# Optimization experiments

Measured on AMD Instinct MI355X. Metric: run time of the kernel, lower is better.

The kernel has to match this reference:

```python
import jax, jax.numpy as jnp
import numpy as np

LN_EPS = 1e-5  # torch nn.LayerNorm default


def layernorm(x, g, b):
    mu = jnp.mean(x, axis=-1, keepdims=True)
    var = jnp.var(x, axis=-1, keepdims=True)
    return (x - mu) * jax.lax.rsqrt(var + LN_EPS) * g + b


def setup_inputs() -> dict:
    key = jax.random.key(0)
    ks = jax.random.split(key, 12)
    B, N, Dn, Dm, E, L = 4, 20000, 64, 128, 160000, 2
    inp = {}
    inp["node_feat"] = jax.random.normal(ks[0], (B, N, Dn), jnp.float32)
    inp["in_W"] = jax.random.normal(ks[1], (Dn, Dm), jnp.float32) * 0.1
    inp["in_b"] = jnp.zeros((Dm,), jnp.float32)
    inp["node_W"] = jax.random.normal(ks[2], (L, 3, Dm, Dm), jnp.float32) * 0.05
    inp["node_b"] = jnp.zeros((L, 3, Dm), jnp.float32)
    inp["edge_W"] = jax.random.normal(ks[3], (L, 2, 16, Dm), jnp.float32) * 0.1
    inp["edge_b"] = jnp.zeros((L, 2, Dm), jnp.float32)
    inp["ln_g"] = jnp.ones((L, Dm), jnp.float32)
    inp["ln_b"] = jnp.zeros((L, Dm), jnp.float32)
    inp["ea0"] = jax.random.normal(ks[4], (E, 16), jnp.float32)
    inp["ea1"] = jax.random.normal(ks[5], (E, 16), jnp.float32)
    inp["ei0"] = jax.random.randint(ks[6], (2, E), 0, N)
    inp["ei1"] = jax.random.randint(ks[7], (2, E), 0, N)
    inp["ei2"] = jax.random.randint(ks[8], (2, E), 0, N)
    return inp


def reference(node_feat, in_W, in_b, node_W, node_b, edge_W, edge_b, ln_g, ln_b,
              ea0, ea1, ei0, ei1, ei2):
    # input projection: [B,N,Dn] -> [B,N,Dm]
    H = node_feat @ in_W + in_b
    edge_idx = [ei0, ei1, ei2]
    edge_attr = [ea0, ea1, None]  # relation 2 has edge_attr_dims == 0 (Identity/skip)
    n_layers = node_W.shape[0]
    for l in range(n_layers):
        agg = jnp.zeros_like(H)
        for r in range(3):
            src, dst = edge_idx[r][0], edge_idx[r][1]
            # gather src nodes per batch then per-relation linear: [B,E,Dm]
            msg = H[:, src] @ node_W[l, r] + node_b[l, r]
            if edge_attr[r] is not None:
                # edge attrs shared across batch -> broadcast add
                msg = msg + (edge_attr[r] @ edge_W[l, r] + edge_b[l, r])[None]
            # scatter-add messages to dst nodes, batched
            agg = agg.at[:, dst].add(msg)
        H = layernorm(H + jax.nn.relu(agg), ln_g[l], ln_b[l])
    return H
```

## Files before the change

### kernel.cpp

```cpp
#include <hip/hip_runtime.h>


#define NNODES 20000
#define NB     4
#define BROWS  (NB * NNODES)
#define DN     64
#define DM     128
#define NE     160000
#define CAP    64
#define LN_EPS 1e-5f
#define KE     448
#define LDW    88

typedef __attribute__((ext_vector_type(8))) short bf16x8;
typedef __attribute__((ext_vector_type(4))) float f32x4;
typedef __attribute__((ext_vector_type(2))) float f32x2;
typedef __attribute__((ext_vector_type(8))) unsigned short u16x8;

__device__ inline float bf2f(unsigned short u) {
    union { unsigned int i; float f; } x; x.i = ((unsigned int)u) << 16; return x.f;
}
__device__ inline unsigned short f2bf(float f) {
    union { float f; unsigned int i; } x; x.f = f;
    unsigned int r = x.i + 0x7FFFu + ((x.i >> 16) & 1u);
    return (unsigned short)(r >> 16);
}
__device__ inline f32x2 bfpair(unsigned int w) {
    union { unsigned int u; float f; } lo, hi;
    lo.u = w << 16; hi.u = w & 0xffff0000u;
    return (f32x2){lo.f, hi.f};
}

__global__ void k_scatter(const int* __restrict__ ei0, const int* __restrict__ ei1,
                          const int* __restrict__ ei2, int* __restrict__ cursor,
                          int* __restrict__ srcs, int* __restrict__ eids) {
    int tid = blockIdx.x * blockDim.x + threadIdx.x;
    if (tid >= 3 * NE) return;
    int r = tid / NE, e = tid - r * NE;
    const int* ei = (r == 0) ? ei0 : ((r == 1) ? ei1 : ei2);
    int src = ei[e], dst = ei[NE + e];
    int p = atomicAdd(&cursor[r * NNODES + dst], 1);
    if (p < CAP) {
        srcs[(r * NNODES + dst) * CAP + p] = src << 8;
        if (r < 2) eids[(r * NNODES + dst) * CAP + p] = e;
    }
}

__global__ __launch_bounds__(256) void k_sgather(const int* __restrict__ deg,
                                                 const int* __restrict__ eids,
                                                 const float* __restrict__ ea0,
                                                 const float* __restrict__ ea1,
                                                 float* __restrict__ S) {
    int task = blockIdx.x * 4 + (threadIdx.x >> 6);
    int r = task / NNODES;
    const float* ea = r ? ea1 : ea0;
    int lane = threadIdx.x & 63;
    int k = lane & 15, sub = lane >> 4;
    int dg = deg[task]; if (dg > CAP) dg = CAP;
    const int* bk = eids + (size_t)task * CAP;
    float acc = 0.f;
    for (int j = sub; j < dg; j += 4) {
        int e = bk[j];
        acc += ea[e * 16 + k];
    }
    acc += __shfl_xor(acc, 16, 64);
    acc += __shfl_xor(acc, 32, 64);
    if (lane < 16) S[(size_t)task * 16 + k] = acc;
}

__global__ __launch_bounds__(256) void k_wprep(const float* __restrict__ nW,
                                               const float* __restrict__ nb,
                                               const float* __restrict__ eW,
                                               const float* __restrict__ eb,
                                               const float* __restrict__ inW,
                                               unsigned short* __restrict__ Wt,
                                               unsigned short* __restrict__ Wp) {
    int lin = blockIdx.x * 256 + threadIdx.x;
    if (lin < 2 * 128 * KE) {
        int l = lin / (128 * KE);
        int rem = lin - l * 128 * KE;
        int n = rem / KE, k = rem - n * KE;
        float v;
        if (k < 384) {
            int r = k >> 7, kk = k & 127;
            v = nW[(((size_t)(l * 3 + r) * 128) + kk) * 128 + n];
        } else {
            int e = k - 384;
            if (e < 3) {
                v = nb[(l * 3 + e) * DM + n];
                if (e < 2) v += eb[(l * 2 + e) * DM + n];
            } else if (e < 35) {
                int r2 = (e - 3) >> 4, j = (e - 3) & 15;
                v = eW[((size_t)((l * 2 + r2) * 16 + j)) * DM + n];
            } else v = 0.f;
        }
        Wt[lin] = f2bf(v);
    } else {
        int i = lin - 2 * 128 * KE;
        int n = i >> 6, k = i & 63;
        Wp[n * 64 + k] = f2bf(inW[(size_t)k * DM + n]);
    }
}

__global__ __launch_bounds__(256) void k_proj(const float* __restrict__ X,
                                              const unsigned short* __restrict__ Wp,
                                              const float* __restrict__ bias,
                                              unsigned short* __restrict__ HB) {
    __shared__ __align__(16) unsigned short As[64][LDW];
    __shared__ __align__(16) unsigned short Bs[128][LDW];
    int t = threadIdx.x;
    int m0 = blockIdx.x * 64;
#pragma unroll
    for (int i = 0; i < 4; ++i) {
        int lin = t + 256 * i;
        int row = lin >> 4, seg = lin & 15;
        float4 v = *(const float4*)(X + (size_t)(m0 + row) * DN + seg * 4);
        ushort4 h; h.x = f2bf(v.x); h.y = f2bf(v.y); h.z = f2bf(v.z); h.w = f2bf(v.w);
        *(ushort4*)&As[row][seg * 4] = h;
    }
#pragma unroll
    for (int i = 0; i < 4; ++i) {
        int lin = t + 256 * i;
        int row = lin >> 3, seg = lin & 7;
        *(uint4*)&Bs[row][seg * 8] = *(const uint4*)(Wp + (size_t)row * 64 + seg * 8);
    }
    __syncthreads();
    int w = t >> 6, lane = t & 63;
    int q = lane >> 4, lm = lane & 15;
    f32x4 acc[8];
#pragma unroll
    for (int ct = 0; ct < 8; ++ct) acc[ct] = (f32x4){0.f, 0.f, 0.f, 0.f};
#pragma unroll
    for (int kt = 0; kt < 2; ++kt) {
        bf16x8 a = *(const bf16x8*)&As[w * 16 + lm][kt * 32 + q * 8];
#pragma unroll
        for (int ct = 0; ct < 8; ++ct) {
            bf16x8 bf = *(const bf16x8*)&Bs[ct * 16 + lm][kt * 32 + q * 8];
            acc[ct] = __builtin_amdgcn_mfma_f32_16x16x32_bf16(a, bf, acc[ct], 0, 0, 0);
        }
    }
#pragma unroll
    for (int reg = 0; reg < 4; ++reg) {
        int row = m0 + w * 16 + q * 4 + reg;
#pragma unroll
        for (int ct = 0; ct < 8; ++ct) {
            int col = ct * 16 + lm;
            HB[(size_t)row * DM + col] = f2bf(acc[ct][reg] + bias[col]);
        }
    }
}

__device__ inline uint4 ld16(const char* __restrict__ base, unsigned off) {
    return *(const uint4*)(base + off);
}
__device__ inline void acc4(f32x2* a, uint4 p0, uint4 p1, uint4 p2, uint4 p3) {
    a[0] += (bfpair(p0.x) + bfpair(p1.x)) + (bfpair(p2.x) + bfpair(p3.x));
    a[1] += (bfpair(p0.y) + bfpair(p1.y)) + (bfpair(p2.y) + bfpair(p3.y));
    a[2] += (bfpair(p0.z) + bfpair(p1.z)) + (bfpair(p2.z) + bfpair(p3.z));
    a[3] += (bfpair(p0.w) + bfpair(p1.w)) + (bfpair(p2.w) + bfpair(p3.w));
}

__device__ inline void gather_rel(const char* __restrict__ HbB, unsigned c16,
                                  const int* __restrict__ bk, int dg, f32x2* a) {
#pragma unroll
    for (int i = 0; i < 4; ++i) a[i] = (f32x2){0.f, 0.f};
    int nb = dg >> 2;
    int j = nb << 2;
    if (nb > 0) {
        int4 s = *(const int4*)bk;
        uint4 p0 = ld16(HbB, (unsigned)s.x + c16);
        uint4 p1 = ld16(HbB, (unsigned)s.y + c16);
        uint4 p2 = ld16(HbB, (unsigned)s.z + c16);
        uint4 p3 = ld16(HbB, (unsigned)s.w + c16);
        for (int b = 1; b < nb; ++b) {
            int4 s2 = *(const int4*)(bk + (b << 2));
            uint4 q0 = ld16(HbB, (unsigned)s2.x + c16);
            uint4 q1 = ld16(HbB, (unsigned)s2.y + c16);
            uint4 q2 = ld16(HbB, (unsigned)s2.z + c16);
            uint4 q3 = ld16(HbB, (unsigned)s2.w + c16);
            acc4(a, p0, p1, p2, p3);
            p0 = q0; p1 = q1; p2 = q2; p3 = q3;
        }
        acc4(a, p0, p1, p2, p3);
    }
    for (; j < dg; ++j) {
        uint4 u = ld16(HbB, (unsigned)bk[j] + c16);
        a[0] += bfpair(u.x); a[1] += bfpair(u.y);
        a[2] += bfpair(u.z); a[3] += bfpair(u.w);
    }
}

__global__ __launch_bounds__(256) void k_spmm(const unsigned short* __restrict__ HB,
                                              const int* __restrict__ deg,
                                              const int* __restrict__ srcs,
                                              const float* __restrict__ S,
                                              unsigned short* __restrict__ G) {
    int blk = blockIdx.x;
    int s = blk & 7;
    int bb = s >> 1;
    int idx = ((blk >> 3) << 1) + (s & 1);
    int n0 = idx * 16;
    int g = threadIdx.x >> 4, lane = threadIdx.x & 15;
    int n = n0 + g;
    unsigned c16 = (unsigned)lane * 16;
    const char* HbB = (const char*)HB + (size_t)bb * NNODES * DM * 2;
    size_t rowbase = ((size_t)(bb * NNODES + n)) * KE;

    int dt0 = deg[n], dt1 = deg[NNODES + n], dt2 = deg[2 * NNODES + n];
    const int* bk0 = srcs + (size_t)n * CAP;
    const int* bk1 = bk0 + (size_t)NNODES * CAP;
    const int* bk2 = bk1 + (size_t)NNODES * CAP;

    f32x2 a[4];
    u16x8 o;

    gather_rel(HbB, c16, bk0, dt0 > CAP ? CAP : dt0, a);
#pragma unroll
    for (int i = 0; i < 4; ++i) { o[2 * i] = f2bf(a[i].x); o[2 * i + 1] = f2bf(a[i].y); }
    *(u16x8*)(G + rowbase + 0 * 128 + lane * 8) = o;

    gather_rel(HbB, c16, bk1, dt1 > CAP ? CAP : dt1, a);
#pragma unroll
    for (int i = 0; i < 4; ++i) { o[2 * i] = f2bf(a[i].x); o[2 * i + 1] = f2bf(a[i].y); }
    *(u16x8*)(G + rowbase + 1 * 128 + lane * 8) = o;

    gather_rel(HbB, c16, bk2, dt2 > CAP ? CAP : dt2, a);
#pragma unroll
    for (int i = 0; i < 4; ++i) { o[2 * i] = f2bf(a[i].x); o[2 * i + 1] = f2bf(a[i].y); }
    *(u16x8*)(G + rowbase + 2 * 128 + lane * 8) = o;

    if (lane < 8) {
        int dt[3] = {dt0, dt1, dt2};
        u16x8 e;
#pragma unroll
        for (int j = 0; j < 8; ++j) {
            int kk = lane * 8 + j;
            float v;
            if (kk < 3)       v = (float)dt[kk];
            else if (kk < 19) v = S[((size_t)(0 * NNODES + n)) * 16 + (kk - 3)];
            else if (kk < 35) v = S[((size_t)(1 * NNODES + n)) * 16 + (kk - 19)];
            else              v = 0.f;
            e[j] = f2bf(v);
        }
        *(u16x8*)(G + rowbase + 384 + lane * 8) = e;
    }
}

__global__ __launch_bounds__(256) void k_gemm_ln(const unsigned short* __restrict__ G,
                                                 const unsigned short* __restrict__ Wt,
                                                 unsigned short* HB,
                                                 const float* __restrict__ lng,
                                                 const float* __restrict__ lnb,
                                                 float* __restrict__ out, int write_f32) {
    __shared__ __align__(16) unsigned short Gs[64][LDW];
    __shared__ __align__(16) unsigned short Ws[128][LDW];
    int t = threadIdx.x;
    int m0 = blockIdx.x * 64;
    int w = t >> 6, lane = t & 63;
    int q = lane >> 4, lm = lane & 15;

    f32x4 acc[8];
#pragma unroll
    for (int ct = 0; ct < 8; ++ct) acc[ct] = (f32x4){0.f, 0.f, 0.f, 0.f};

    for (int kc = 0; kc < 7; ++kc) {
#pragma unroll
        for (int i = 0; i < 2; ++i) {
            int lin = t + 256 * i;
            int row = lin >> 3, seg = lin & 7;
            *(uint4*)&Gs[row][seg * 8] =
                *(const uint4*)(G + (size_t)(m0 + row) * KE + kc * 64 + seg * 8);
        }
#pragma unroll
        for (int i = 0; i < 4; ++i) {
            int lin = t + 256 * i;
            int row = lin >> 3, seg = lin & 7;
            *(uint4*)&Ws[row][seg * 8] =
                *(const uint4*)(Wt + (size_t)row * KE + kc * 64 + seg * 8);
        }
        __syncthreads();
#pragma unroll
        for (int kt = 0; kt < 2; ++kt) {
            bf16x8 a = *(const bf16x8*)&Gs[w * 16 + lm][kt * 32 + q * 8];
#pragma unroll
            for (int ct = 0; ct < 8; ++ct) {
                bf16x8 bf = *(const bf16x8*)&Ws[ct * 16 + lm][kt * 32 + q * 8];
                acc[ct] = __builtin_amdgcn_mfma_f32_16x16x32_bf16(a, bf, acc[ct], 0, 0, 0);
            }
        }
        __syncthreads();
    }

    float gc[8], bc[8];
#pragma unroll
    for (int ct = 0; ct < 8; ++ct) {
        int col = ct * 16 + lm;
        gc[ct] = lng[col]; bc[ct] = lnb[col];
    }
#pragma unroll
    for (int reg = 0; reg < 4; ++reg) {
        size_t row = (size_t)m0 + w * 16 + q * 4 + reg;
        float xv[8];
        float s1 = 0.f, s2 = 0.f;
#pragma unroll
        for (int ct = 0; ct < 8; ++ct) {
            int col = ct * 16 + lm;
            float h = bf2f(HB[row * DM + col]);
            float v = h + fmaxf(acc[ct][reg], 0.f);
            xv[ct] = v; s1 += v; s2 += v * v;
        }
#pragma unroll
        for (int m = 1; m <= 8; m <<= 1) {
            s1 += __shfl_xor(s1, m, 64);
            s2 += __shfl_xor(s2, m, 64);
        }
        float mu  = s1 * (1.f / 128.f);
        float var = s2 * (1.f / 128.f) - mu * mu;
        float inv = rsqrtf(var + LN_EPS);
        if (write_f32) {
#pragma unroll
            for (int ct = 0; ct < 8; ++ct) {
                int col = ct * 16 + lm;
                out[row * DM + col] = (xv[ct] - mu) * inv * gc[ct] + bc[ct];
            }
        } else {
#pragma unroll
            for (int ct = 0; ct < 8; ++ct) {
                int col = ct * 16 + lm;
                HB[row * DM + col] = f2bf((xv[ct] - mu) * inv * gc[ct] + bc[ct]);
            }
        }
    }
}

extern "C" void kernel_launch(void* const* d_in, const int* in_sizes, int n_in,
                              void* d_out, int out_size, void* d_ws, size_t ws_size,
                              hipStream_t stream) {
    const float* node_feat = (const float*)d_in[0];
    const float* in_W   = (const float*)d_in[1];
    const float* in_b   = (const float*)d_in[2];
    const float* node_W = (const float*)d_in[3];
    const float* node_b = (const float*)d_in[4];
    const float* edge_W = (const float*)d_in[5];
    const float* edge_b = (const float*)d_in[6];
    const float* ln_g   = (const float*)d_in[7];
    const float* ln_b   = (const float*)d_in[8];
    const float* ea0    = (const float*)d_in[9];
    const float* ea1    = (const float*)d_in[10];
    const int*   ei0    = (const int*)d_in[11];
    const int*   ei1    = (const int*)d_in[12];
    const int*   ei2    = (const int*)d_in[13];
    float* out = (float*)d_out;

    char* ws = (char*)d_ws;
    size_t off = 0;
    auto alloc = [&](size_t bytes) -> void* {
        void* p = ws + off;
        off = (off + bytes + 255) & ~(size_t)255;
        return p;
    };
    unsigned short* HB     = (unsigned short*)alloc((size_t)BROWS * DM * 2);
    unsigned short* G      = (unsigned short*)alloc((size_t)BROWS * KE * 2);
    int*            cursor = (int*)alloc((size_t)3 * NNODES * 4);
    float*          S      = (float*)alloc((size_t)2 * NNODES * 16 * 4);
    int*            srcs   = (int*)alloc((size_t)3 * NNODES * CAP * 4);
    int*            eids   = (int*)alloc((size_t)2 * NNODES * CAP * 4);
    unsigned short* Wt     = (unsigned short*)alloc((size_t)2 * 128 * KE * 2);
    unsigned short* Wp     = (unsigned short*)alloc((size_t)128 * 64 * 2);

    hipMemsetAsync(cursor, 0, (size_t)3 * NNODES * 4, stream);

    k_scatter<<<(3 * NE + 255) / 256, 256, 0, stream>>>(ei0, ei1, ei2, cursor, srcs, eids);
    k_sgather<<<(2 * NNODES) / 4, 256, 0, stream>>>(cursor, eids, ea0, ea1, S);
    k_wprep<<<480, 256, 0, stream>>>(node_W, node_b, edge_W, edge_b, in_W, Wt, Wp);
    k_proj<<<BROWS / 64, 256, 0, stream>>>(node_feat, Wp, in_b, HB);

    for (int l = 0; l < 2; ++l) {
        k_spmm<<<5000, 256, 0, stream>>>(HB, cursor, srcs, S, G);
        k_gemm_ln<<<BROWS / 64, 256, 0, stream>>>(G, Wt + (size_t)l * 128 * KE, HB,
                                                  ln_g + (size_t)l * DM, ln_b + (size_t)l * DM,
                                                  out, l == 1);
    }
}
```

Baseline: 335.8 us.

## Split SpMM gather across feature halves and add nontemporal loads/stores

The gather-sum kernel now splits each node's 128-wide feature row into two 64-column halves handled by separate blocks, so the grid doubles and each lane loads 8 bytes per neighbor instead of 16. This raises parallelism and memory-level concurrency for the latency-bound gather. Index-list loads, G stores, and G loads in the GEMM now use nontemporal hints to avoid polluting cache with streaming data. The cost is narrower loads, index lists read twice, and two blocks sharing each node's G row.

```diff
diff --git a/kernel.cpp b/kernel.cpp
--- a/kernel.cpp
+++ b/kernel.cpp
@@ -16,6 +16,10 @@
 typedef __attribute__((ext_vector_type(4))) float f32x4;
 typedef __attribute__((ext_vector_type(2))) float f32x2;
 typedef __attribute__((ext_vector_type(8))) unsigned short u16x8;
+typedef __attribute__((ext_vector_type(4))) unsigned short u16x4;
+typedef __attribute__((ext_vector_type(4))) int i32x4;
+typedef __attribute__((ext_vector_type(2))) unsigned int u32x2;
+typedef __attribute__((ext_vector_type(4))) unsigned int u32x4;
 
 __device__ inline float bf2f(unsigned short u) {
     union { unsigned int i; float f; } x; x.i = ((unsigned int)u) << 16; return x.f;
@@ -150,43 +154,30 @@
     }
 }
 
-__device__ inline uint4 ld16(const char* __restrict__ base, unsigned off) {
-    return *(const uint4*)(base + off);
-}
-__device__ inline void acc4(f32x2* a, uint4 p0, uint4 p1, uint4 p2, uint4 p3) {
-    a[0] += (bfpair(p0.x) + bfpair(p1.x)) + (bfpair(p2.x) + bfpair(p3.x));
-    a[1] += (bfpair(p0.y) + bfpair(p1.y)) + (bfpair(p2.y) + bfpair(p3.y));
-    a[2] += (bfpair(p0.z) + bfpair(p1.z)) + (bfpair(p2.z) + bfpair(p3.z));
-    a[3] += (bfpair(p0.w) + bfpair(p1.w)) + (bfpair(p2.w) + bfpair(p3.w));
-}
-
-__device__ inline void gather_rel(const char* __restrict__ HbB, unsigned c16,
-                                  const int* __restrict__ bk, int dg, f32x2* a) {
-#pragma unroll
-    for (int i = 0; i < 4; ++i) a[i] = (f32x2){0.f, 0.f};
-    int nb = dg >> 2;
-    int j = nb << 2;
-    if (nb > 0) {
-        int4 s = *(const int4*)bk;
-        uint4 p0 = ld16(HbB, (unsigned)s.x + c16);
-        uint4 p1 = ld16(HbB, (unsigned)s.y + c16);
-        uint4 p2 = ld16(HbB, (unsigned)s.z + c16);
-        uint4 p3 = ld16(HbB, (unsigned)s.w + c16);
-        for (int b = 1; b < nb; ++b) {
-            int4 s2 = *(const int4*)(bk + (b << 2));
-            uint4 q0 = ld16(HbB, (unsigned)s2.x + c16);
-            uint4 q1 = ld16(HbB, (unsigned)s2.y + c16);
-            uint4 q2 = ld16(HbB, (unsigned)s2.z + c16);
-            uint4 q3 = ld16(HbB, (unsigned)s2.w + c16);
-            acc4(a, p0, p1, p2, p3);
-            p0 = q0; p1 = q1; p2 = q2; p3 = q3;
-        }
-        acc4(a, p0, p1, p2, p3);
+__device__ inline void gather_rel_h(const char* __restrict__ HbB2, unsigned c8,
+                                    const int* __restrict__ bk, int dg, f32x2* a) {
+    a[0] = (f32x2){0.f, 0.f};
+    a[1] = (f32x2){0.f, 0.f};
+    int j = 0;
+    if (dg >= 4) {
+        i32x4 s4 = __builtin_nontemporal_load((const i32x4*)bk);
+        while (j + 3 < dg) {
+            i32x4 nxt = s4;
+            if (j + 7 < dg) nxt = __builtin_nontemporal_load((const i32x4*)(bk + j + 4));
+            u32x2 u0 = *(const u32x2*)(HbB2 + ((unsigned)s4.x + c8));
+            u32x2 u1 = *(const u32x2*)(HbB2 + ((unsigned)s4.y + c8));
+            u32x2 u2 = *(const u32x2*)(HbB2 + ((unsigned)s4.z + c8));
+            u32x2 u3 = *(const u32x2*)(HbB2 + ((unsigned)s4.w + c8));
+            a[0] += (bfpair(u0.x) + bfpair(u1.x)) + (bfpair(u2.x) + bfpair(u3.x));
+            a[1] += (bfpair(u0.y) + bfpair(u1.y)) + (bfpair(u2.y) + bfpair(u3.y));
+            j += 4;
+            s4 = nxt;
+        }
     }
     for (; j < dg; ++j) {
-        uint4 u = ld16(HbB, (unsigned)bk[j] + c16);
-        a[0] += bfpair(u.x); a[1] += bfpair(u.y);
-        a[2] += bfpair(u.z); a[3] += bfpair(u.w);
+        u32x2 u = *(const u32x2*)(HbB2 + ((unsigned)bk[j] + c8));
+        a[0] += bfpair(u.x);
+        a[1] += bfpair(u.y);
     }
 }
 
@@ -198,12 +189,13 @@
     int blk = blockIdx.x;
     int s = blk & 7;
     int bb = s >> 1;
-    int idx = ((blk >> 3) << 1) + (s & 1);
+    int hh = s & 1;
+    int idx = blk >> 3;
     int n0 = idx * 16;
     int g = threadIdx.x >> 4, lane = threadIdx.x & 15;
     int n = n0 + g;
-    unsigned c16 = (unsigned)lane * 16;
-    const char* HbB = (const char*)HB + (size_t)bb * NNODES * DM * 2;
+    unsigned c8 = (unsigned)lane * 8;
+    const char* HbB2 = (const char*)HB + (size_t)bb * NNODES * DM * 2 + hh * 128;
     size_t rowbase = ((size_t)(bb * NNODES + n)) * KE;
 
     int dt0 = deg[n], dt1 = deg[NNODES + n], dt2 = deg[2 * NNODES + n];
@@ -211,25 +203,22 @@
     const int* bk1 = bk0 + (size_t)NNODES * CAP;
     const int* bk2 = bk1 + (size_t)NNODES * CAP;
 
-    f32x2 a[4];
-    u16x8 o;
-
-    gather_rel(HbB, c16, bk0, dt0 > CAP ? CAP : dt0, a);
-#pragma unroll
-    for (int i = 0; i < 4; ++i) { o[2 * i] = f2bf(a[i].x); o[2 * i + 1] = f2bf(a[i].y); }
-    *(u16x8*)(G + rowbase + 0 * 128 + lane * 8) = o;
-
-    gather_rel(HbB, c16, bk1, dt1 > CAP ? CAP : dt1, a);
-#pragma unroll
-    for (int i = 0; i < 4; ++i) { o[2 * i] = f2bf(a[i].x); o[2 * i + 1] = f2bf(a[i].y); }
-    *(u16x8*)(G + rowbase + 1 * 128 + lane * 8) = o;
-
-    gather_rel(HbB, c16, bk2, dt2 > CAP ? CAP : dt2, a);
-#pragma unroll
-    for (int i = 0; i < 4; ++i) { o[2 * i] = f2bf(a[i].x); o[2 * i + 1] = f2bf(a[i].y); }
-    *(u16x8*)(G + rowbase + 2 * 128 + lane * 8) = o;
-
-    if (lane < 8) {
+    f32x2 a[2];
+    u16x4 o;
+
+    gather_rel_h(HbB2, c8, bk0, dt0 > CAP ? CAP : dt0, a);
+    o[0] = f2bf(a[0].x); o[1] = f2bf(a[0].y); o[2] = f2bf(a[1].x); o[3] = f2bf(a[1].y);
+    __builtin_nontemporal_store(o, (u16x4*)(G + rowbase + 0 * 128 + hh * 64 + lane * 4));
+
+    gather_rel_h(HbB2, c8, bk1, dt1 > CAP ? CAP : dt1, a);
+    o[0] = f2bf(a[0].x); o[1] = f2bf(a[0].y); o[2] = f2bf(a[1].x); o[3] = f2bf(a[1].y);
+    __builtin_nontemporal_store(o, (u16x4*)(G + rowbase + 1 * 128 + hh * 64 + lane * 4));
+
+    gather_rel_h(HbB2, c8, bk2, dt2 > CAP ? CAP : dt2, a);
+    o[0] = f2bf(a[0].x); o[1] = f2bf(a[0].y); o[2] = f2bf(a[1].x); o[3] = f2bf(a[1].y);
+    __builtin_nontemporal_store(o, (u16x4*)(G + rowbase + 2 * 128 + hh * 64 + lane * 4));
+
+    if (hh == 0 && lane < 8) {
         int dt[3] = {dt0, dt1, dt2};
         u16x8 e;
 #pragma unroll
@@ -242,7 +231,7 @@
             else              v = 0.f;
             e[j] = f2bf(v);
         }
-        *(u16x8*)(G + rowbase + 384 + lane * 8) = e;
+        __builtin_nontemporal_store(e, (u16x8*)(G + rowbase + 384 + lane * 8));
     }
 }
 
@@ -268,8 +257,9 @@
         for (int i = 0; i < 2; ++i) {
             int lin = t + 256 * i;
             int row = lin >> 3, seg = lin & 7;
-            *(uint4*)&Gs[row][seg * 8] =
-                *(const uint4*)(G + (size_t)(m0 + row) * KE + kc * 64 + seg * 8);
+            u32x4 v = __builtin_nontemporal_load(
+                (const u32x4*)(G + (size_t)(m0 + row) * KE + kc * 64 + seg * 8));
+            *(u32x4*)&Gs[row][seg * 8] = v;
         }
 #pragma unroll
         for (int i = 0; i < 4; ++i) {
@@ -376,7 +366,7 @@
     k_proj<<<BROWS / 64, 256, 0, stream>>>(node_feat, Wp, in_b, HB);
 
     for (int l = 0; l < 2; ++l) {
-        k_spmm<<<5000, 256, 0, stream>>>(HB, cursor, srcs, S, G);
+        k_spmm<<<10000, 256, 0, stream>>>(HB, cursor, srcs, S, G);
         k_gemm_ln<<<BROWS / 64, 256, 0, stream>>>(G, Wt + (size_t)l * 128 * KE, HB,
                                                   ln_g + (size_t)l * DM, ln_b + (size_t)l * DM,
                                                   out, l == 1);
```

Result: slower. 448.5 us (+33.5%).
